# Performance work log

Hardware: AMD Instinct MI355X
Metric: run time of the kernel (lower is better)

## Reference

```python
import jax, jax.numpy as jnp
import numpy as np

B, C, W, H = 4, 256, 64, 64


def setup_inputs() -> dict:
    key = jax.random.key(0)
    ks = jax.random.split(key, 10)
    s = 1.0 / np.sqrt(C)  # fan-in style scale for 1x1 conv weights
    return {
        "x": jax.random.normal(ks[0], (B, C, W, H), dtype=jnp.float32),
        "Wq": jax.random.normal(ks[1], (C, C), dtype=jnp.float32) * s,
        "bq": jax.random.normal(ks[2], (C,), dtype=jnp.float32) * 0.02,
        "Wk": jax.random.normal(ks[3], (C, C), dtype=jnp.float32) * s,
        "bk": jax.random.normal(ks[4], (C,), dtype=jnp.float32) * 0.02,
        "Wv": jax.random.normal(ks[5], (C, C), dtype=jnp.float32) * s,
        "bv": jax.random.normal(ks[6], (C,), dtype=jnp.float32) * 0.02,
        "rel_h": jax.random.normal(ks[7], (1, C, H, 1), dtype=jnp.float32),
        "rel_w": jax.random.normal(ks[8], (1, C, 1, W), dtype=jnp.float32),
        # gamma is initialized to 0 in the original; use a nonzero value so the
        # attention branch actually contributes (otherwise out == x).
        "gamma": jnp.full((1,), 0.5, dtype=jnp.float32),
    }


def reference(x, Wq, bq, Wk, bk, Wv, bv, rel_h, rel_w, gamma):
    Bz, Cc, Ww, Hh = x.shape
    N = Ww * Hh
    xf = x.reshape(Bz, Cc, N)  # [B, C, N]

    # 1x1 convs == per-pixel linear projections over channels
    q = jnp.einsum('oc,bcn->bno', Wq, xf) + bq            # [B, N, C]
    k = jnp.einsum('oc,bcn->bon', Wk, xf) + bk[:, None]   # [B, C, N]
    v = jnp.einsum('oc,bcn->bon', Wv, xf) + bv[:, None]   # [B, C, N]

    # relative position bias: (rel_h + rel_w) -> [C, N], projected by q
    pos = (rel_h + rel_w).reshape(Cc, N)                  # [C, N]
    energy = jnp.einsum('bnc,bcm->bnm', q, k) + q @ pos   # [B, N, N]

    att = jax.nn.softmax(energy, axis=-1)                 # [B, N, N]

    # out[b,c,m] = sum_n v[b,c,n] * att[b,m,n]
    out = jnp.einsum('bcn,bmn->bcm', v, att).reshape(Bz, Cc, Ww, Hh)
    return gamma * out + x
```

## Files before the change

### kernel.cpp

```cpp
#include <hip/hip_runtime.h>
#include <stdint.h>

#define N_TOK 4096
#define C_DIM 256
#define NSPLIT 2

typedef __attribute__((ext_vector_type(8))) short short8;
typedef __attribute__((ext_vector_type(8))) _Float16 half8;
typedef __attribute__((ext_vector_type(4))) float floatx4;
typedef __attribute__((ext_vector_type(4))) unsigned short ushort4v;

__device__ __forceinline__ unsigned short bf16_rne(float f) {
    union { float f; unsigned int u; } v; v.f = f;
    unsigned int u = v.u;
    unsigned int rounded = u + 0x7FFFu + ((u >> 16) & 1u);
    return (unsigned short)(rounded >> 16);
}
__device__ __forceinline__ float bf16_to_f(unsigned short h) {
    union { unsigned int u; float f; } v; v.u = ((unsigned int)h) << 16;
    return v.f;
}
__device__ __forceinline__ void split_bf16(float f, unsigned short& h, unsigned short& l) {
    h = bf16_rne(f);
    l = bf16_rne(f - bf16_to_f(h));
}
__device__ __forceinline__ unsigned short f2h(float f) {
    union { _Float16 h; unsigned short u; } v; v.h = (_Float16)f; return v.u;
}
__device__ __forceinline__ float h2f(unsigned short u) {
    union { unsigned short u; _Float16 h; } v; v.u = u; return (float)v.h;
}
__device__ __forceinline__ void g2l16(const void* g, void* l) {
    __builtin_amdgcn_global_load_lds(
        (const __attribute__((address_space(1))) void*)g,
        (__attribute__((address_space(3))) void*)l, 16, 0, 0);
}

__global__ __launch_bounds__(256) void prep_kernel(
    const float* __restrict__ x,
    const float* __restrict__ Wq, const float* __restrict__ Wk, const float* __restrict__ Wv,
    unsigned short* __restrict__ Xhi, unsigned short* __restrict__ Xlo,
    unsigned short* __restrict__ Whi, unsigned short* __restrict__ Wlo)
{
    const int t = threadIdx.x;
    if (blockIdx.x >= 1024) {
        const int pj = blockIdx.x - 1024;
        const float* W = (pj == 0) ? Wq : (pj == 1) ? Wk : Wv;
        unsigned short* dh = Whi + pj * 65536;
        unsigned short* dl = Wlo + pj * 65536;
        for (int it = 0; it < 64; it++) {
            const int idx = it * 1024 + t * 4;
            const float4 w = *(const float4*)&W[idx];
            unsigned short h0, l0, h1, l1, h2, l2, h3, l3;
            split_bf16(w.x, h0, l0); split_bf16(w.y, h1, l1);
            split_bf16(w.z, h2, l2); split_bf16(w.w, h3, l3);
            ushort4v vh; vh[0] = h0; vh[1] = h1; vh[2] = h2; vh[3] = h3;
            ushort4v vl; vl[0] = l0; vl[1] = l1; vl[2] = l2; vl[3] = l3;
            *(ushort4v*)&dh[idx] = vh;
            *(ushort4v*)&dl[idx] = vl;
        }
        return;
    }
    __shared__ float Xs[64 * 65];
    const int b  = blockIdx.x >> 8;
    const int ct = (blockIdx.x >> 6) & 3;
    const int nt = blockIdx.x & 63;
    const int c0 = ct * 64, n0 = nt * 64;
    {
        const int nch = t & 15, cr = t >> 4;
#pragma unroll
        for (int pass = 0; pass < 4; pass++) {
            const int c = pass * 16 + cr;
            const float4 v = *(const float4*)&x[((size_t)(b * C_DIM + c0 + c)) * N_TOK + n0 + nch * 4];
            float* row = &Xs[c * 65 + nch * 4];
            row[0] = v.x; row[1] = v.y; row[2] = v.z; row[3] = v.w;
        }
    }
    __syncthreads();
    {
        const int n = t >> 2, cc = t & 3;
        short8 vh0, vl0, vh1, vl1;
#pragma unroll
        for (int i = 0; i < 8; i++) {
            unsigned short h, l;
            split_bf16(Xs[(cc * 16 + i) * 65 + n], h, l);
            vh0[i] = (short)h; vl0[i] = (short)l;
        }
#pragma unroll
        for (int i = 0; i < 8; i++) {
            unsigned short h, l;
            split_bf16(Xs[(cc * 16 + 8 + i) * 65 + n], h, l);
            vh1[i] = (short)h; vl1[i] = (short)l;
        }
        const size_t off = ((size_t)b * N_TOK + n0 + n) * C_DIM + c0 + cc * 16;
        *(short8*)&Xhi[off] = vh0; *(short8*)&Xhi[off + 8] = vh1;
        *(short8*)&Xlo[off] = vl0; *(short8*)&Xlo[off + 8] = vl1;
    }
}

__global__ __launch_bounds__(256) void proj_kernel(
    const unsigned short* __restrict__ Xhi, const unsigned short* __restrict__ Xlo,
    const unsigned short* __restrict__ Whi, const unsigned short* __restrict__ Wlo,
    const float* __restrict__ bq, const float* __restrict__ bk, const float* __restrict__ bv,
    const float* __restrict__ relh, const float* __restrict__ relw,
    unsigned short* __restrict__ Qh,
    unsigned short* __restrict__ Kh,
    unsigned short* __restrict__ Vh)
{
    __shared__ unsigned short SM[20480];
    unsigned short* Ah = SM;
    unsigned short* Al = SM + 2048;
    unsigned short* Bh = SM + 4096;
    unsigned short* Bl = SM + 12288;

    const int t    = threadIdx.x;
    const int wave = t >> 6;
    const int lane = t & 63;
    const int l15  = lane & 15;
    const int quad = lane >> 4;

    const int bp   = blockIdx.x >> 6;
    const int proj = bp % 3;
    const int b    = bp / 3;
    const int n0   = (blockIdx.x & 63) * 64;

    const unsigned short* Xh = Xhi + ((size_t)b * N_TOK + n0) * C_DIM;
    const unsigned short* Xl = Xlo + ((size_t)b * N_TOK + n0) * C_DIM;
    const unsigned short* Wh = Whi + proj * 65536;
    const unsigned short* Wl = Wlo + proj * 65536;
    const float* bias = (proj == 0) ? bq : (proj == 1) ? bk : bv;
    const bool needlo = (proj < 2);

    floatx4 acc[16];
#pragma unroll
    for (int i = 0; i < 16; i++) acc[i] = (floatx4){0.f, 0.f, 0.f, 0.f};

    for (int c0 = 0; c0 < 256; c0 += 32) {
        {
            const int lr = lane >> 2, cp = lane & 3;
            const int key = (lr ^ (lr >> 2)) & 3;
            const int r = wave * 16 + lr;
            g2l16(Xh + (size_t)r * C_DIM + c0 + (cp ^ key) * 8, &Ah[wave * 512]);
            if (needlo) g2l16(Xl + (size_t)r * C_DIM + c0 + (cp ^ key) * 8, &Al[wave * 512]);
#pragma unroll
            for (int p = 0; p < 4; p++) {
                const int rb = (p * 4 + wave) * 16;
                const int rr = rb + lr;
                g2l16(Wh + (size_t)rr * 256 + c0 + (cp ^ key) * 8, &Bh[rb * 32]);
                if (needlo) g2l16(Wl + (size_t)rr * 256 + c0 + (cp ^ key) * 8, &Bl[rb * 32]);
            }
        }
        __syncthreads();

        const int akey = (l15 ^ (l15 >> 2)) & 3;
        const int arow = (wave * 16 + l15) * 32 + ((quad ^ akey) * 8);
        const short8 a_h = *(const short8*)&Ah[arow];
        short8 a_l;
        if (needlo) a_l = *(const short8*)&Al[arow];
#pragma unroll
        for (int ot = 0; ot < 16; ot++) {
            const int brow = (ot * 16 + l15) * 32 + ((quad ^ akey) * 8);
            const short8 b_h = *(const short8*)&Bh[brow];
            acc[ot] = __builtin_amdgcn_mfma_f32_16x16x32_bf16(a_h, b_h, acc[ot], 0, 0, 0);
            if (needlo) {
                const short8 b_l = *(const short8*)&Bl[brow];
                acc[ot] = __builtin_amdgcn_mfma_f32_16x16x32_bf16(a_l, b_h, acc[ot], 0, 0, 0);
                acc[ot] = __builtin_amdgcn_mfma_f32_16x16x32_bf16(a_h, b_l, acc[ot], 0, 0, 0);
            }
        }
        __syncthreads();
    }

    const int h0 = n0 >> 6;
    if (proj == 0) {
        unsigned short* Og = Qh + ((size_t)b * N_TOK + n0) * C_DIM;
#pragma unroll
        for (int ot = 0; ot < 16; ot++) {
            const int o = ot * 16 + l15;
            const float bs = bias[o];
#pragma unroll
            for (int r = 0; r < 4; r++) {
                const int nl = wave * 16 + quad * 4 + r;
                Og[(size_t)nl * C_DIM + o] = f2h(acc[ot][r] + bs);
            }
        }
    } else if (proj == 1) {
        unsigned short* Og = Kh + ((size_t)b * N_TOK + n0) * C_DIM;
#pragma unroll
        for (int ot = 0; ot < 16; ot++) {
            const int o = ot * 16 + l15;
            const float bs = bias[o];
            const float ph = relh[o * 64 + h0];
#pragma unroll
            for (int r = 0; r < 4; r++) {
                const int nl = wave * 16 + quad * 4 + r;
                Og[(size_t)nl * C_DIM + o] = f2h(acc[ot][r] + bs + ph + relw[o * 64 + nl]);
            }
        }
    } else {
        unsigned short* Vt = SM;
#pragma unroll
        for (int ot = 0; ot < 16; ot++) {
            const int o = ot * 16 + l15;
            const float bs = bias[o];
            const unsigned int u0 = (unsigned int)f2h(acc[ot][0] + bs) |
                                    ((unsigned int)f2h(acc[ot][1] + bs) << 16);
            const unsigned int u1 = (unsigned int)f2h(acc[ot][2] + bs) |
                                    ((unsigned int)f2h(acc[ot][3] + bs) << 16);
            uint2 uv; uv.x = u0; uv.y = u1;
            *(uint2*)&Vt[o * 72 + wave * 16 + quad * 4] = uv;
        }
        __syncthreads();
        const int ch   = t & 7;
        const int orow = t >> 3;
#pragma unroll
        for (int pass = 0; pass < 8; pass++) {
            const int o = pass * 32 + orow;
            const short8 vv = *(const short8*)&Vt[o * 72 + ch * 8];
            *(short8*)&Vh[((size_t)b * C_DIM + o) * N_TOK + n0 + ch * 8] = vv;
        }
    }
}

__global__ __launch_bounds__(256, 2) void flash_kernel(
    const unsigned short* __restrict__ Qg,
    const unsigned short* __restrict__ Kg,
    const unsigned short* __restrict__ Vg,
    unsigned short* __restrict__ Op,
    float* __restrict__ Lm)
{
    __shared__ unsigned short Ks[64 * 256];
    __shared__ unsigned short Vs[256 * 64];
    __shared__ unsigned short Pt[4 * 16 * 72];
    __shared__ float abuf[4][16];

    const int t    = threadIdx.x;
    const int wave = t >> 6;
    const int lane = t & 63;
    const int l15  = lane & 15;
    const int quad = lane >> 4;
    const int lk   = l15 & 7;

    const int bid = blockIdx.x;
    const int b   = bid & 3;
    const int s   = (bid >> 2) & 1;
    const int qt  = bid >> 3;

    const unsigned short* Kb = Kg + (size_t)b * N_TOK * C_DIM;
    const unsigned short* Vb = Vg + (size_t)b * C_DIM * N_TOK;

    half8 qf[8];
    const int qrow = qt * 64 + wave * 16 + l15;
    {
        const unsigned short* Qrow = Qg + ((size_t)b * N_TOK + qrow) * C_DIM;
#pragma unroll
        for (int ct = 0; ct < 8; ct++)
            qf[ct] = *(const half8*)&Qrow[ct * 32 + quad * 8];
    }

    floatx4 oacc[16];
#pragma unroll
    for (int i = 0; i < 16; i++) oacc[i] = (floatx4){0.f, 0.f, 0.f, 0.f};
    float m_i[4] = {-1e30f, -1e30f, -1e30f, -1e30f};
    float l_i[4] = {0.f, 0.f, 0.f, 0.f};

    unsigned short* Ptw = Pt + wave * 16 * 72;
    const int jbase = s * 2048;

    {
        const int lr = lane >> 5, cp = lane & 31;
#pragma unroll
        for (int p = 0; p < 8; p++) {
            const int jl = wave * 16 + p * 2 + lr;
            g2l16(Kb + (size_t)(jbase + jl) * C_DIM + (cp ^ (jl & 7)) * 8,
                  &Ks[(wave * 16 + p * 2) * 256]);
        }
    }

    for (int ti = 0; ti < 32; ti++) {
        const int j0 = jbase + ti * 64;

        __syncthreads();

        {
            const int lr = lane >> 3, cp = lane & 7;
#pragma unroll
            for (int p = 0; p < 8; p++) {
                const int ob = (p * 4 + wave) * 8;
                const int o  = ob + lr;
                g2l16(Vb + (size_t)o * N_TOK + j0 + (cp ^ (o & 7)) * 8, &Vs[ob * 64]);
            }
        }

        floatx4 sv[4];
#pragma unroll
        for (int jt = 0; jt < 4; jt++) {
            floatx4 a = (floatx4){0.f, 0.f, 0.f, 0.f};
#pragma unroll
            for (int ct = 0; ct < 8; ct++) {
                const half8 kb = *(const half8*)&Ks[(jt * 16 + l15) * 256 + (((ct * 4 + quad) ^ lk) * 8)];
                a = __builtin_amdgcn_mfma_f32_16x16x32_f16(qf[ct], kb, a, 0, 0, 0);
            }
            sv[jt] = a;
        }

        float alpha[4];
#pragma unroll
        for (int r = 0; r < 4; r++) {
            float mx = fmaxf(fmaxf(sv[0][r], sv[1][r]), fmaxf(sv[2][r], sv[3][r]));
            mx = fmaxf(mx, __shfl_xor(mx, 1));
            mx = fmaxf(mx, __shfl_xor(mx, 2));
            mx = fmaxf(mx, __shfl_xor(mx, 4));
            mx = fmaxf(mx, __shfl_xor(mx, 8));
            const float mn = fmaxf(m_i[r], mx);
            alpha[r] = __expf(m_i[r] - mn);
            m_i[r] = mn;
            float ps = 0.f;
#pragma unroll
            for (int jt = 0; jt < 4; jt++) {
                const float p = __expf(sv[jt][r] - mn);
                sv[jt][r] = p;
                ps += p;
            }
            ps += __shfl_xor(ps, 1);
            ps += __shfl_xor(ps, 2);
            ps += __shfl_xor(ps, 4);
            ps += __shfl_xor(ps, 8);
            l_i[r] = l_i[r] * alpha[r] + ps;
        }

#pragma unroll
        for (int jt = 0; jt < 4; jt++) {
#pragma unroll
            for (int r = 0; r < 4; r++)
                Ptw[(quad * 4 + r) * 72 + jt * 16 + l15] = f2h(sv[jt][r]);
        }
        if (l15 == 0)
            *(float4*)&abuf[wave][quad * 4] = make_float4(alpha[0], alpha[1], alpha[2], alpha[3]);
        const half8 pf0 = *(const half8*)&Ptw[l15 * 72 + quad * 8];
        const half8 pf1 = *(const half8*)&Ptw[l15 * 72 + 32 + quad * 8];
        const float am = abuf[wave][l15];
#pragma unroll
        for (int ot = 0; ot < 16; ot++) {
            oacc[ot][0] *= am; oacc[ot][1] *= am; oacc[ot][2] *= am; oacc[ot][3] *= am;
        }

        __syncthreads();

        if (ti < 31) {
            const int lr = lane >> 5, cp = lane & 31;
#pragma unroll
            for (int p = 0; p < 8; p++) {
                const int jl = wave * 16 + p * 2 + lr;
                g2l16(Kb + (size_t)(j0 + 64 + jl) * C_DIM + (cp ^ (jl & 7)) * 8,
                      &Ks[(wave * 16 + p * 2) * 256]);
            }
        }

#pragma unroll
        for (int ot = 0; ot < 16; ot++) {
            const int row = (ot * 16 + l15) * 64;
            const half8 av0 = *(const half8*)&Vs[row + ((quad ^ lk) * 8)];
            const half8 av1 = *(const half8*)&Vs[row + (((4 + quad) ^ lk) * 8)];
            oacc[ot] = __builtin_amdgcn_mfma_f32_16x16x32_f16(av0, pf0, oacc[ot], 0, 0, 0);
            oacc[ot] = __builtin_amdgcn_mfma_f32_16x16x32_f16(av1, pf1, oacc[ot], 0, 0, 0);
        }
    }

    unsigned short* Ob = Op + ((size_t)(s * 4 + b) * C_DIM) * N_TOK;
    const int n = qt * 64 + wave * 16 + l15;
#pragma unroll
    for (int ot = 0; ot < 16; ot++) {
#pragma unroll
        for (int r = 0; r < 4; r++) {
            const int c = ot * 16 + quad * 4 + r;
            Ob[(size_t)c * N_TOK + n] = f2h(oacc[ot][r]);
        }
    }
    if (l15 == 0) {
        const size_t nb = (size_t)(s * 4 + b) * N_TOK + qt * 64 + wave * 16 + quad * 4;
#pragma unroll
        for (int r = 0; r < 4; r++)
            *(float2*)&Lm[(nb + r) * 2] = make_float2(m_i[r], l_i[r]);
    }
}

__global__ __launch_bounds__(256) void merge_kernel(
    const unsigned short* __restrict__ Op,
    const float* __restrict__ Lm,
    const float* __restrict__ x,
    const float* __restrict__ gamma,
    float* __restrict__ out)
{
    const int blk = blockIdx.x;
    const int b   = blk >> 10;
    const int c   = (blk >> 2) & 255;
    const int nq  = blk & 3;
    const int n0  = nq * 1024 + threadIdx.x * 4;

    const size_t NEo = (size_t)4 * C_DIM * N_TOK;
    const size_t obase = ((size_t)b * C_DIM + c) * N_TOK + n0;

    float ms[NSPLIT][4], ls[NSPLIT][4], os[NSPLIT][4];
#pragma unroll
    for (int s = 0; s < NSPLIT; s++) {
        const uint2 u = *(const uint2*)&Op[s * NEo + obase];
        os[s][0] = h2f((unsigned short)(u.x & 0xffff));
        os[s][1] = h2f((unsigned short)(u.x >> 16));
        os[s][2] = h2f((unsigned short)(u.y & 0xffff));
        os[s][3] = h2f((unsigned short)(u.y >> 16));
        const float* Lms = Lm + (size_t)(s * 4 + b) * N_TOK * 2;
        const float4 A0 = *(const float4*)&Lms[n0 * 2];
        const float4 A1 = *(const float4*)&Lms[n0 * 2 + 4];
        ms[s][0] = A0.x; ls[s][0] = A0.y;
        ms[s][1] = A0.z; ls[s][1] = A0.w;
        ms[s][2] = A1.x; ls[s][2] = A1.y;
        ms[s][3] = A1.z; ls[s][3] = A1.w;
    }
    const float4 xv = *(const float4*)&x[obase];
    const float xin[4] = {xv.x, xv.y, xv.z, xv.w};
    const float g = gamma[0];

    float4 res;
    float* rp = (float*)&res;
#pragma unroll
    for (int i = 0; i < 4; i++) {
        float M = ms[0][i];
#pragma unroll
        for (int s = 1; s < NSPLIT; s++) M = fmaxf(M, ms[s][i]);
        float osum = 0.f, lsum = 0.f;
#pragma unroll
        for (int s = 0; s < NSPLIT; s++) {
            const float w = __expf(ms[s][i] - M);
            osum += w * os[s][i];
            lsum += w * ls[s][i];
        }
        rp[i] = g * osum / lsum + xin[i];
    }
    *(float4*)&out[obase] = res;
}

extern "C" void kernel_launch(void* const* d_in, const int* in_sizes, int n_in,
                              void* d_out, int out_size, void* d_ws, size_t ws_size,
                              hipStream_t stream) {
    const float* x     = (const float*)d_in[0];
    const float* Wq    = (const float*)d_in[1];
    const float* bq    = (const float*)d_in[2];
    const float* Wk    = (const float*)d_in[3];
    const float* bk    = (const float*)d_in[4];
    const float* Wv    = (const float*)d_in[5];
    const float* bv    = (const float*)d_in[6];
    const float* relh  = (const float*)d_in[7];
    const float* relw  = (const float*)d_in[8];
    const float* gamma = (const float*)d_in[9];
    float* out = (float*)d_out;

    const size_t NE = (size_t)4 * N_TOK * C_DIM;

    unsigned short* Op  = (unsigned short*)d_ws;
    unsigned short* Xhi = Op;
    unsigned short* Xlo = Op + NE;
    unsigned short* Whi = Op + (size_t)NSPLIT * NE;
    unsigned short* Wlo = Whi + 3 * 65536;
    unsigned short* Qh  = Wlo + 3 * 65536;
    unsigned short* Kh  = Qh + NE;
    unsigned short* Vh  = Kh + NE;
    float* Lm = (float*)(Vh + NE);

    hipLaunchKernelGGL(prep_kernel, dim3(1027), dim3(256), 0, stream,
                       x, Wq, Wk, Wv, Xhi, Xlo, Whi, Wlo);
    hipLaunchKernelGGL(proj_kernel, dim3(768), dim3(256), 0, stream,
                       Xhi, Xlo, Whi, Wlo, bq, bk, bv, relh, relw, Qh, Kh, Vh);
    hipLaunchKernelGGL(flash_kernel, dim3(512), dim3(256), 0, stream,
                       Qh, Kh, Vh, Op, Lm);
    hipLaunchKernelGGL(merge_kernel, dim3(4096), dim3(256), 0, stream,
                       Op, Lm, x, gamma, out);
}
```

Before: 263.4 us.

## Give each wave 32 query rows, read V from global, split keys four ways

The flash kernel now processes two 16-row query groups per wave, so a block covers 128 queries. Each staged K tile is reused twice as many times, and the key range is split across 4 partitions instead of 2, which keeps the grid size the same. V is no longer staged in LDS: MFMA operands are loaded straight from global memory. The P tile goes through a swizzled LDS layout, and the per-row rescale factor is passed by a lane shuffle instead of an LDS buffer. The cost is roughly double the accumulator and Q registers, which may cause spills or lower occupancy. V traffic becomes redundant across waves and depends on cache hits.

```diff
diff --git a/kernel.cpp b/kernel.cpp
--- a/kernel.cpp
+++ b/kernel.cpp
@@ -3,7 +3,7 @@
 
 #define N_TOK 4096
 #define C_DIM 256
-#define NSPLIT 2
+#define NSPLIT 4
 
 typedef __attribute__((ext_vector_type(8))) short short8;
 typedef __attribute__((ext_vector_type(8))) _Float16 half8;
@@ -34,6 +34,13 @@
     __builtin_amdgcn_global_load_lds(
         (const __attribute__((address_space(1))) void*)g,
         (__attribute__((address_space(3))) void*)l, 16, 0, 0);
+}
+__device__ __forceinline__ float sel4(const float v[4], int r) {
+    float x = v[0];
+    x = (r == 1) ? v[1] : x;
+    x = (r == 2) ? v[2] : x;
+    x = (r == 3) ? v[3] : x;
+    return x;
 }
 
 __global__ __launch_bounds__(256) void prep_kernel(
@@ -230,9 +237,7 @@
     float* __restrict__ Lm)
 {
     __shared__ unsigned short Ks[64 * 256];
-    __shared__ unsigned short Vs[256 * 64];
-    __shared__ unsigned short Pt[4 * 16 * 72];
-    __shared__ float abuf[4][16];
+    __shared__ unsigned short Pt[4 * 32 * 64];
 
     const int t    = threadIdx.x;
     const int wave = t >> 6;
@@ -243,29 +248,33 @@
 
     const int bid = blockIdx.x;
     const int b   = bid & 3;
-    const int s   = (bid >> 2) & 1;
-    const int qt  = bid >> 3;
+    const int s   = (bid >> 2) & 3;
+    const int qt  = bid >> 4;
 
     const unsigned short* Kb = Kg + (size_t)b * N_TOK * C_DIM;
     const unsigned short* Vb = Vg + (size_t)b * C_DIM * N_TOK;
 
-    half8 qf[8];
-    const int qrow = qt * 64 + wave * 16 + l15;
-    {
+    half8 qf[2][8];
+#pragma unroll
+    for (int mg = 0; mg < 2; mg++) {
+        const int qrow = qt * 128 + wave * 32 + mg * 16 + l15;
         const unsigned short* Qrow = Qg + ((size_t)b * N_TOK + qrow) * C_DIM;
 #pragma unroll
         for (int ct = 0; ct < 8; ct++)
-            qf[ct] = *(const half8*)&Qrow[ct * 32 + quad * 8];
-    }
-
-    floatx4 oacc[16];
-#pragma unroll
-    for (int i = 0; i < 16; i++) oacc[i] = (floatx4){0.f, 0.f, 0.f, 0.f};
-    float m_i[4] = {-1e30f, -1e30f, -1e30f, -1e30f};
-    float l_i[4] = {0.f, 0.f, 0.f, 0.f};
-
-    unsigned short* Ptw = Pt + wave * 16 * 72;
-    const int jbase = s * 2048;
+            qf[mg][ct] = *(const half8*)&Qrow[ct * 32 + quad * 8];
+    }
+
+    floatx4 oacc[2][16];
+#pragma unroll
+    for (int mg = 0; mg < 2; mg++)
+#pragma unroll
+        for (int i = 0; i < 16; i++) oacc[mg][i] = (floatx4){0.f, 0.f, 0.f, 0.f};
+    float m_i[2][4] = {{-1e30f, -1e30f, -1e30f, -1e30f}, {-1e30f, -1e30f, -1e30f, -1e30f}};
+    float l_i[2][4] = {{0.f, 0.f, 0.f, 0.f}, {0.f, 0.f, 0.f, 0.f}};
+
+    unsigned short* Ptw = Pt + wave * 32 * 64;
+    const int jbase = s * 1024;
+    const int bsrc = ((l15 >> 2) << 4) | (l15 & 3);
 
     {
         const int lr = lane >> 5, cp = lane & 31;
@@ -277,77 +286,66 @@
         }
     }
 
-    for (int ti = 0; ti < 32; ti++) {
+    for (int ti = 0; ti < 16; ti++) {
         const int j0 = jbase + ti * 64;
 
         __syncthreads();
 
-        {
-            const int lr = lane >> 3, cp = lane & 7;
-#pragma unroll
-            for (int p = 0; p < 8; p++) {
-                const int ob = (p * 4 + wave) * 8;
-                const int o  = ob + lr;
-                g2l16(Vb + (size_t)o * N_TOK + j0 + (cp ^ (o & 7)) * 8, &Vs[ob * 64]);
-            }
-        }
-
-        floatx4 sv[4];
-#pragma unroll
-        for (int jt = 0; jt < 4; jt++) {
-            floatx4 a = (floatx4){0.f, 0.f, 0.f, 0.f};
-#pragma unroll
-            for (int ct = 0; ct < 8; ct++) {
-                const half8 kb = *(const half8*)&Ks[(jt * 16 + l15) * 256 + (((ct * 4 + quad) ^ lk) * 8)];
-                a = __builtin_amdgcn_mfma_f32_16x16x32_f16(qf[ct], kb, a, 0, 0, 0);
-            }
-            sv[jt] = a;
-        }
-
-        float alpha[4];
-#pragma unroll
-        for (int r = 0; r < 4; r++) {
-            float mx = fmaxf(fmaxf(sv[0][r], sv[1][r]), fmaxf(sv[2][r], sv[3][r]));
-            mx = fmaxf(mx, __shfl_xor(mx, 1));
-            mx = fmaxf(mx, __shfl_xor(mx, 2));
-            mx = fmaxf(mx, __shfl_xor(mx, 4));
-            mx = fmaxf(mx, __shfl_xor(mx, 8));
-            const float mn = fmaxf(m_i[r], mx);
-            alpha[r] = __expf(m_i[r] - mn);
-            m_i[r] = mn;
-            float ps = 0.f;
+        float am[2];
+#pragma unroll
+        for (int mg = 0; mg < 2; mg++) {
+            floatx4 sv[4];
 #pragma unroll
             for (int jt = 0; jt < 4; jt++) {
-                const float p = __expf(sv[jt][r] - mn);
-                sv[jt][r] = p;
-                ps += p;
-            }
-            ps += __shfl_xor(ps, 1);
-            ps += __shfl_xor(ps, 2);
-            ps += __shfl_xor(ps, 4);
-            ps += __shfl_xor(ps, 8);
-            l_i[r] = l_i[r] * alpha[r] + ps;
-        }
-
-#pragma unroll
-        for (int jt = 0; jt < 4; jt++) {
-#pragma unroll
-            for (int r = 0; r < 4; r++)
-                Ptw[(quad * 4 + r) * 72 + jt * 16 + l15] = f2h(sv[jt][r]);
-        }
-        if (l15 == 0)
-            *(float4*)&abuf[wave][quad * 4] = make_float4(alpha[0], alpha[1], alpha[2], alpha[3]);
-        const half8 pf0 = *(const half8*)&Ptw[l15 * 72 + quad * 8];
-        const half8 pf1 = *(const half8*)&Ptw[l15 * 72 + 32 + quad * 8];
-        const float am = abuf[wave][l15];
-#pragma unroll
-        for (int ot = 0; ot < 16; ot++) {
-            oacc[ot][0] *= am; oacc[ot][1] *= am; oacc[ot][2] *= am; oacc[ot][3] *= am;
+                floatx4 a = (floatx4){0.f, 0.f, 0.f, 0.f};
+#pragma unroll
+                for (int ct = 0; ct < 8; ct++) {
+                    const half8 kb = *(const half8*)&Ks[(jt * 16 + l15) * 256 + (((ct * 4 + quad) ^ lk) * 8)];
+                    a = __builtin_amdgcn_mfma_f32_16x16x32_f16(qf[mg][ct], kb, a, 0, 0, 0);
+                }
+                sv[jt] = a;
+            }
+
+            float alpha[4];
+#pragma unroll
+            for (int r = 0; r < 4; r++) {
+                float mx = fmaxf(fmaxf(sv[0][r], sv[1][r]), fmaxf(sv[2][r], sv[3][r]));
+                mx = fmaxf(mx, __shfl_xor(mx, 1));
+                mx = fmaxf(mx, __shfl_xor(mx, 2));
+                mx = fmaxf(mx, __shfl_xor(mx, 4));
+                mx = fmaxf(mx, __shfl_xor(mx, 8));
+                const float mn = fmaxf(m_i[mg][r], mx);
+                alpha[r] = __expf(m_i[mg][r] - mn);
+                m_i[mg][r] = mn;
+                float ps = 0.f;
+#pragma unroll
+                for (int jt = 0; jt < 4; jt++) {
+                    const float p = __expf(sv[jt][r] - mn);
+                    sv[jt][r] = p;
+                    ps += p;
+                }
+                ps += __shfl_xor(ps, 1);
+                ps += __shfl_xor(ps, 2);
+                ps += __shfl_xor(ps, 4);
+                ps += __shfl_xor(ps, 8);
+                l_i[mg][r] = l_i[mg][r] * alpha[r] + ps;
+            }
+
+#pragma unroll
+            for (int jt = 0; jt < 4; jt++) {
+#pragma unroll
+                for (int r = 0; r < 4; r++) {
+                    const int m  = mg * 16 + quad * 4 + r;
+                    const int cj = jt * 2 + (l15 >> 3);
+                    Ptw[m * 64 + ((cj ^ (m & 7)) << 3) + (l15 & 7)] = f2h(sv[jt][r]);
+                }
+            }
+            am[mg] = __shfl(sel4(alpha, l15 & 3), bsrc);
         }
 
         __syncthreads();
 
-        if (ti < 31) {
+        if (ti < 15) {
             const int lr = lane >> 5, cp = lane & 31;
 #pragma unroll
             for (int p = 0; p < 8; p++) {
@@ -357,31 +355,53 @@
             }
         }
 
-#pragma unroll
-        for (int ot = 0; ot < 16; ot++) {
-            const int row = (ot * 16 + l15) * 64;
-            const half8 av0 = *(const half8*)&Vs[row + ((quad ^ lk) * 8)];
-            const half8 av1 = *(const half8*)&Vs[row + (((4 + quad) ^ lk) * 8)];
-            oacc[ot] = __builtin_amdgcn_mfma_f32_16x16x32_f16(av0, pf0, oacc[ot], 0, 0, 0);
-            oacc[ot] = __builtin_amdgcn_mfma_f32_16x16x32_f16(av1, pf1, oacc[ot], 0, 0, 0);
+        half8 pf[2][2];
+#pragma unroll
+        for (int mg = 0; mg < 2; mg++) {
+            const int m = mg * 16 + l15;
+#pragma unroll
+            for (int hf = 0; hf < 2; hf++)
+                pf[mg][hf] = *(const half8*)&Ptw[m * 64 + (((hf * 4 + quad) ^ (l15 & 7)) << 3)];
+        }
+
+#pragma unroll
+        for (int mg = 0; mg < 2; mg++)
+#pragma unroll
+            for (int ot = 0; ot < 16; ot++) {
+                oacc[mg][ot][0] *= am[mg]; oacc[mg][ot][1] *= am[mg];
+                oacc[mg][ot][2] *= am[mg]; oacc[mg][ot][3] *= am[mg];
+            }
+
+#pragma unroll
+        for (int ot = 0; ot < 16; ot++) {
+            const unsigned short* vrow = Vb + (size_t)(ot * 16 + l15) * N_TOK + j0;
+            const half8 av0 = *(const half8*)&vrow[quad * 8];
+            const half8 av1 = *(const half8*)&vrow[32 + quad * 8];
+            oacc[0][ot] = __builtin_amdgcn_mfma_f32_16x16x32_f16(av0, pf[0][0], oacc[0][ot], 0, 0, 0);
+            oacc[0][ot] = __builtin_amdgcn_mfma_f32_16x16x32_f16(av1, pf[0][1], oacc[0][ot], 0, 0, 0);
+            oacc[1][ot] = __builtin_amdgcn_mfma_f32_16x16x32_f16(av0, pf[1][0], oacc[1][ot], 0, 0, 0);
+            oacc[1][ot] = __builtin_amdgcn_mfma_f32_16x16x32_f16(av1, pf[1][1], oacc[1][ot], 0, 0, 0);
         }
     }
 
     unsigned short* Ob = Op + ((size_t)(s * 4 + b) * C_DIM) * N_TOK;
-    const int n = qt * 64 + wave * 16 + l15;
-#pragma unroll
-    for (int ot = 0; ot < 16; ot++) {
-#pragma unroll
-        for (int r = 0; r < 4; r++) {
-            const int c = ot * 16 + quad * 4 + r;
-            Ob[(size_t)c * N_TOK + n] = f2h(oacc[ot][r]);
-        }
-    }
-    if (l15 == 0) {
-        const size_t nb = (size_t)(s * 4 + b) * N_TOK + qt * 64 + wave * 16 + quad * 4;
-#pragma unroll
-        for (int r = 0; r < 4; r++)
-            *(float2*)&Lm[(nb + r) * 2] = make_float2(m_i[r], l_i[r]);
+#pragma unroll
+    for (int mg = 0; mg < 2; mg++) {
+        const int n = qt * 128 + wave * 32 + mg * 16 + l15;
+#pragma unroll
+        for (int ot = 0; ot < 16; ot++) {
+#pragma unroll
+            for (int r = 0; r < 4; r++) {
+                const int c = ot * 16 + quad * 4 + r;
+                Ob[(size_t)c * N_TOK + n] = f2h(oacc[mg][ot][r]);
+            }
+        }
+        if (l15 == 0) {
+            const size_t nb = (size_t)(s * 4 + b) * N_TOK + qt * 128 + wave * 32 + mg * 16 + quad * 4;
+#pragma unroll
+            for (int r = 0; r < 4; r++)
+                *(float2*)&Lm[(nb + r) * 2] = make_float2(m_i[mg][r], l_i[mg][r]);
+        }
     }
 }
 
```

New measurement: 544.1 us. +106.5%, slower.
